# Kernel optimization log

Hardware: AMD Instinct MI355X
Metric: run time of the kernel (lower is better)

Reference implementation:

```python
import jax, jax.numpy as jnp
import numpy as np
from jax import lax

L, T, DM, DH = 4, 4096, 2048, 1024
MAX_PHASE = 6.28
EPS = 1e-5


def setup_inputs() -> dict:
    key = jax.random.key(0)
    ks = jax.random.split(key, 16)
    # LRU initializers (r_min=0, r_max=1)
    u1 = jax.random.uniform(ks[0], (L, DH))
    nu_log = jnp.log(-0.5 * jnp.log(u1))
    u2 = jax.random.uniform(ks[1], (L, DH))
    theta_log = jnp.log(MAX_PHASE * u2)
    abs_lam = jnp.exp(-jnp.exp(nu_log))  # |lambda|
    gamma_log = jnp.log(jnp.sqrt(1.0 - abs_lam ** 2))
    B_re = jax.random.normal(ks[2], (L, DH, DM)) / np.sqrt(2 * DM)
    B_im = jax.random.normal(ks[3], (L, DH, DM)) / np.sqrt(2 * DM)
    C_re = jax.random.normal(ks[4], (L, DM, DH)) / np.sqrt(DH)
    C_im = jax.random.normal(ks[5], (L, DM, DH)) / np.sqrt(DH)
    D = jax.random.normal(ks[6], (L, DM))
    bound = 1.0 / np.sqrt(DM)
    enc_w = jax.random.uniform(ks[7], (DM, DM), minval=-bound, maxval=bound)
    enc_b = jax.random.uniform(ks[8], (DM,), minval=-bound, maxval=bound)
    out1_w = jax.random.uniform(ks[9], (L, DM, DM), minval=-bound, maxval=bound)
    out1_b = jax.random.uniform(ks[10], (L, DM), minval=-bound, maxval=bound)
    out2_w = jax.random.uniform(ks[11], (L, DM, DM), minval=-bound, maxval=bound)
    out2_b = jax.random.uniform(ks[12], (L, DM), minval=-bound, maxval=bound)
    norm_w = jnp.ones((L, DM))
    norm_b = jnp.zeros((L, DM))
    x = jax.random.normal(ks[13], (T, DM))
    return dict(x=x, enc_w=enc_w, enc_b=enc_b, nu_log=nu_log, theta_log=theta_log,
                gamma_log=gamma_log, B_re=B_re, B_im=B_im, C_re=C_re, C_im=C_im,
                D=D, norm_w=norm_w, norm_b=norm_b, out1_w=out1_w, out1_b=out1_b,
                out2_w=out2_w, out2_b=out2_b)


def _lru(xn, nu, th, gl, br, bi, cr, ci, d):
    # xn: (T, DM) real -> (T, DM) real
    lam = jnp.exp(-jnp.exp(nu) + 1j * jnp.exp(th))          # (DH,) complex
    B_norm = (br + 1j * bi) * jnp.exp(gl)[:, None]           # (DH, DM)
    Bu = xn.astype(B_norm.dtype) @ B_norm.T                  # (T, DH) complex
    a = jnp.broadcast_to(lam, Bu.shape)
    def combine(e1, e2):
        a1, b1 = e1
        a2, b2 = e2
        return a1 * a2, a2 * b1 + b2
    _, h = lax.associative_scan(combine, (a, Bu), axis=0)    # h_t = lam*h_{t-1} + Bu_t
    C = cr + 1j * ci
    return (h @ C.T).real + xn * d


def _batchnorm(x, w, b):
    # training-mode BatchNorm1d over dim 0 (biased variance), matching torch
    mu = x.mean(axis=0)
    var = jnp.mean((x - mu) ** 2, axis=0)
    return (x - mu) / jnp.sqrt(var + EPS) * w + b


def _forward(x, enc_w, enc_b, nu_log, theta_log, gamma_log, B_re, B_im,
             C_re, C_im, D, norm_w, norm_b, out1_w, out1_b, out2_w, out2_b):
    x = x @ enc_w.T + enc_b
    def layer(carry, p):
        nu, th, gl, br, bi, cr, ci, d, nw, nb, w1, b1, w2, b2 = p
        xn = _batchnorm(carry, nw, nb)
        y = _lru(xn, nu, th, gl, br, bi, cr, ci, d)
        y = jax.nn.gelu(y, approximate=False)
        y = (y @ w1.T + b1) * jax.nn.sigmoid(y @ w2.T + b2)
        return carry + y, None
    x, _ = lax.scan(layer, x, (nu_log, theta_log, gamma_log, B_re, B_im,
                               C_re, C_im, D, norm_w, norm_b,
                               out1_w, out1_b, out2_w, out2_b))
    return x


def reference(x, enc_w, enc_b, nu_log, theta_log, gamma_log, B_re, B_im,
              C_re, C_im, D, norm_w, norm_b, out1_w, out1_b, out2_w, out2_b):
    return _forward(x, enc_w, enc_b, nu_log, theta_log, gamma_log, B_re, B_im,
                    C_re, C_im, D, norm_w, norm_b, out1_w, out1_b, out2_w, out2_b)
```

## Files before the change

kernel.cpp:

```cpp
#include <hip/hip_runtime.h>
#include <stdint.h>
#include <math.h>


#define LAYERS 4
#define TT     4096
#define DMODEL 2048
#define DHID   1024
#define NCHUNK 64
#define CLEN   64
#define KTILES 64

typedef unsigned short ushort_t;
typedef __attribute__((ext_vector_type(8))) _Float16 half8;
typedef __attribute__((ext_vector_type(4))) float    f32x4;

__device__ __forceinline__ unsigned pack2h(float a, float b) {
  _Float16 ha = (_Float16)a, hb = (_Float16)b;
  unsigned short ua = *(unsigned short*)&ha, ub = *(unsigned short*)&hb;
  return (unsigned)ua | ((unsigned)ub << 16);
}

__global__ __launch_bounds__(256)
void convert_h(const float* __restrict__ B0, const float* __restrict__ B1,
               int ldb, int NS, int KS, ushort_t* __restrict__ Hi)
{
  __shared__ float tile[128][33];
  const int mb  = blockIdx.x;
  const int kb  = blockIdx.y;
  const int tid = threadIdx.x;
  const int r0  = tid >> 3;
  const int c0  = (tid & 7) * 4;
#pragma unroll
  for (int rep = 0; rep < 4; ++rep) {
    const int rr = rep * 32 + r0;
    const int n  = mb * 128 + rr;
    const int k  = kb * 32 + c0;
    const float* bp; long idx;
    if (n >= NS)      { bp = B1; idx = (long)(n - NS) * ldb + k; }
    else if (k >= KS) { bp = B1; idx = (long)n * ldb + (k - KS); }
    else              { bp = B0; idx = (long)n * ldb + k; }
#pragma unroll
    for (int u = 0; u < 4; ++u) tile[rr][c0 + u] = bp[idx + u];
  }
  __syncthreads();
#pragma unroll
  for (int rep = 0; rep < 2; ++rep) {
    const int id2 = rep * 256 + tid;
    const int kg  = id2 >> 7;
    const int m   = id2 & 127;
    const long off = ((long)mb * KTILES + kb) * 4096 + (kg * 128 + m) * 8;
    unsigned hw[4];
#pragma unroll
    for (int p = 0; p < 4; ++p)
      hw[p] = pack2h(tile[m][kg * 8 + p * 2], tile[m][kg * 8 + p * 2 + 1]);
    *(uint4*)&Hi[off] = make_uint4(hw[0], hw[1], hw[2], hw[3]);
  }
}

__global__ __launch_bounds__(256)
void bn_convert(const float* __restrict__ carry, const float* __restrict__ stats,
                const float* __restrict__ nw, const float* __restrict__ nb,
                float* __restrict__ act, ushort_t* __restrict__ Hi)
{
  __shared__ float tile[128][33];
  const int mb  = blockIdx.x;
  const int kb  = blockIdx.y;
  const int tid = threadIdx.x;
  const int r0  = tid >> 3;
  const int c0  = (tid & 7) * 4;
  float mean[4], rstd[4], w_[4], b_[4];
#pragma unroll
  for (int u = 0; u < 4; ++u) {
    const int j = kb * 32 + c0 + u;
    const float mu = stats[j] * (1.0f / TT);
    const float va = fmaxf(stats[DMODEL + j] * (1.0f / TT) - mu * mu, 0.0f);
    mean[u] = mu; rstd[u] = rsqrtf(va + 1e-5f);
    w_[u] = nw[j]; b_[u] = nb[j];
  }
#pragma unroll
  for (int rep = 0; rep < 4; ++rep) {
    const int rr  = rep * 32 + r0;
    const long base = (long)(mb * 128 + rr) * 2048 + kb * 32 + c0;
#pragma unroll
    for (int u = 0; u < 4; ++u) {
      const float v = (carry[base + u] - mean[u]) * rstd[u] * w_[u] + b_[u];
      tile[rr][c0 + u] = v;
      act[base + u] = v;
    }
  }
  __syncthreads();
#pragma unroll
  for (int rep = 0; rep < 2; ++rep) {
    const int id2 = rep * 256 + tid;
    const int kg  = id2 >> 7;
    const int m   = id2 & 127;
    const long off = ((long)mb * KTILES + kb) * 4096 + (kg * 128 + m) * 8;
    unsigned hw[4];
#pragma unroll
    for (int p = 0; p < 4; ++p)
      hw[p] = pack2h(tile[m][kg * 8 + p * 2], tile[m][kg * 8 + p * 2 + 1]);
    *(uint4*)&Hi[off] = make_uint4(hw[0], hw[1], hw[2], hw[3]);
  }
}

__global__ __launch_bounds__(256)
void e1_convert(const float* __restrict__ y, const float* __restrict__ xn,
                const float* __restrict__ d, ushort_t* __restrict__ Hi)
{
  __shared__ float tile[128][33];
  const int mb  = blockIdx.x;
  const int kb  = blockIdx.y;
  const int tid = threadIdx.x;
  const int r0  = tid >> 3;
  const int c0  = (tid & 7) * 4;
  float dv[4];
#pragma unroll
  for (int u = 0; u < 4; ++u) dv[u] = d[kb * 32 + c0 + u];
#pragma unroll
  for (int rep = 0; rep < 4; ++rep) {
    const int rr  = rep * 32 + r0;
    const long base = (long)(mb * 128 + rr) * 2048 + kb * 32 + c0;
#pragma unroll
    for (int u = 0; u < 4; ++u) {
      const float v = y[base + u] + xn[base + u] * dv[u];
      tile[rr][c0 + u] = 0.5f * v * (1.0f + erff(v * 0.70710678118654752440f));
    }
  }
  __syncthreads();
#pragma unroll
  for (int rep = 0; rep < 2; ++rep) {
    const int id2 = rep * 256 + tid;
    const int kg  = id2 >> 7;
    const int m   = id2 & 127;
    const long off = ((long)mb * KTILES + kb) * 4096 + (kg * 128 + m) * 8;
    unsigned hw[4];
#pragma unroll
    for (int p = 0; p < 4; ++p)
      hw[p] = pack2h(tile[m][kg * 8 + p * 2], tile[m][kg * 8 + p * 2 + 1]);
    *(uint4*)&Hi[off] = make_uint4(hw[0], hw[1], hw[2], hw[3]);
  }
}

#define GLDS(gp, lp) __builtin_amdgcn_global_load_lds( \
    (__attribute__((address_space(1))) void*)(void*)(gp), \
    (__attribute__((address_space(3))) void*)(lp), 16, 0, 0)

__global__ __launch_bounds__(256)
void gemm_mfma(const ushort_t* __restrict__ Ahi, const ushort_t* __restrict__ Bhi,
               float* __restrict__ C, const float* __restrict__ bias,
               int epi, const float* __restrict__ aux)
{
  __shared__ ushort_t S[2][16384];
  const int tid  = threadIdx.x;
  const int lane = tid & 63;
  const int wid  = tid >> 6;
  const int wm   = wid >> 1;
  const int wn   = wid & 1;

  const int bid = blockIdx.y * gridDim.x + blockIdx.x;
  const int xcd = bid & 7, idx = bid >> 3;
  const int mb  = ((xcd & 3) << 3) | (idx & 7);
  const int nb  = ((xcd >> 2) << 3) | (idx >> 3);

  f32x4 acc[4][4];
#pragma unroll
  for (int i = 0; i < 4; ++i)
#pragma unroll
    for (int j = 0; j < 4; ++j) acc[i][j] = (f32x4){0.f, 0.f, 0.f, 0.f};

  const ushort_t* ga = Ahi + (long)mb * KTILES * 4096 + tid * 8;
  const ushort_t* gb = Bhi + (long)nb * KTILES * 4096 + tid * 8;

  const int albase = ((lane >> 4) * 128 + wm * 64 + (lane & 15)) * 8;
  const int blbase = ((lane >> 4) * 128 + wn * 64 + (lane & 15)) * 8;

  half8 A0[4], B0[4], A1[4], B1[4];

#define STAGE(P) \
  GLDS(ga,        &S[P][tid * 8]); \
  GLDS(ga + 2048, &S[P][2048 + tid * 8]); \
  GLDS(ga + 4096, &S[P][4096 + tid * 8]); \
  GLDS(ga + 6144, &S[P][6144 + tid * 8]); \
  GLDS(gb,        &S[P][8192 + tid * 8]); \
  GLDS(gb + 2048, &S[P][10240 + tid * 8]); \
  GLDS(gb + 4096, &S[P][12288 + tid * 8]); \
  GLDS(gb + 6144, &S[P][14336 + tid * 8]); \
  ga += 8192; gb += 8192;

#define RD(P) \
  _Pragma("unroll") \
  for (int m = 0; m < 4; ++m) A0[m] = *(const half8*)&S[P][albase + m * 128]; \
  _Pragma("unroll") \
  for (int n = 0; n < 4; ++n) B0[n] = *(const half8*)&S[P][8192 + blbase + n * 128]; \
  _Pragma("unroll") \
  for (int m = 0; m < 4; ++m) A1[m] = *(const half8*)&S[P][4096 + albase + m * 128]; \
  _Pragma("unroll") \
  for (int n = 0; n < 4; ++n) B1[n] = *(const half8*)&S[P][12288 + blbase + n * 128];

#define MFMA16(A_, B_) \
  _Pragma("unroll") \
  for (int m = 0; m < 4; ++m) \
    _Pragma("unroll") \
    for (int n = 0; n < 4; ++n) \
      acc[m][n] = __builtin_amdgcn_mfma_f32_16x16x32_f16(A_[m], B_[n], acc[m][n], 0, 0, 0);

#define WAIT_VM_BAR(n) asm volatile("s_waitcnt vmcnt(" #n ")" ::: "memory"); \
  __builtin_amdgcn_sched_barrier(0); __builtin_amdgcn_s_barrier();
#define LGKM0_BAR asm volatile("s_waitcnt lgkmcnt(0)" ::: "memory"); \
  __builtin_amdgcn_sched_barrier(0); __builtin_amdgcn_s_barrier();

#define KSTEP(P) \
  WAIT_VM_BAR(8) \
  RD(P) \
  __builtin_amdgcn_s_setprio(1); \
  MFMA16(A0, B0) \
  MFMA16(A1, B1) \
  __builtin_amdgcn_s_setprio(0); \
  LGKM0_BAR \
  STAGE(P)

  STAGE(0)
  STAGE(1)
  for (int it = 0; it < 15; ++it) {
    KSTEP(0)
    KSTEP(1)
  }
  WAIT_VM_BAR(8)
  RD(0)
  __builtin_amdgcn_s_setprio(1);
  MFMA16(A0, B0)
  MFMA16(A1, B1)
  __builtin_amdgcn_s_setprio(0);
  WAIT_VM_BAR(0)
  RD(1)
  __builtin_amdgcn_s_setprio(1);
  MFMA16(A0, B0)
  MFMA16(A1, B1)
  __builtin_amdgcn_s_setprio(0);
#undef STAGE
#undef RD
#undef MFMA16
#undef WAIT_VM_BAR
#undef LGKM0_BAR
#undef KSTEP

  const int cn = lane & 15;
  const int cr = (lane >> 4) * 4;
#pragma unroll
  for (int m = 0; m < 4; ++m) {
    const long row = (long)mb * 128 + wm * 64 + m * 16 + cr;
#pragma unroll
    for (int n = 0; n < 4; ++n) {
      const int col = nb * 128 + wn * 64 + n * 16 + cn;
      const float bv = bias ? bias[col] : 0.0f;
      if (epi == 0) {
#pragma unroll
        for (int q = 0; q < 4; ++q)
          C[(row + q) * 2048 + col] = acc[m][n][q] + bv;
      } else if (epi == 1) {
#pragma unroll
        for (int q = 0; q < 4; ++q)
          C[(row + q) * 2048 + col] = 1.0f / (1.0f + expf(-(acc[m][n][q] + bv)));
      } else {
#pragma unroll
        for (int q = 0; q < 4; ++q) {
          const long idx2 = (row + q) * 2048 + col;
          C[idx2] += (acc[m][n][q] + bv) * aux[idx2];
        }
      }
    }
  }
}

__global__ __launch_bounds__(256)
void gemm_dual(const ushort_t* __restrict__ Ahi, const ushort_t* __restrict__ B1t,
               const ushort_t* __restrict__ B2t,
               float* __restrict__ carry, const float* __restrict__ b1,
               const float* __restrict__ b2)
{
  __shared__ ushort_t S[3][8192];
  const int tid  = threadIdx.x;
  const int lane = tid & 63;
  const int wid  = tid >> 6;
  const int wm   = wid >> 1;
  const int wn   = wid & 1;

  const int bid = blockIdx.y * gridDim.x + blockIdx.x;
  const int xcd = bid & 7, idx = bid >> 3;
  const int mb  = ((xcd & 3) << 3) | (idx & 7);
  const int nbb = ((xcd >> 2) << 4) | (idx >> 3);

  f32x4 acc1[4][2], acc2[4][2];
#pragma unroll
  for (int i = 0; i < 4; ++i)
#pragma unroll
    for (int j = 0; j < 2; ++j) {
      acc1[i][j] = (f32x4){0.f, 0.f, 0.f, 0.f};
      acc2[i][j] = (f32x4){0.f, 0.f, 0.f, 0.f};
    }

  const int nt = nbb >> 1;
  const int hb = nbb & 1;

  const ushort_t* ga = Ahi + (long)mb * KTILES * 4096 + tid * 8;
  const long boff = ((tid >> 6) * 128 + hb * 64 + (tid & 63)) * 8;
  const ushort_t* g1 = B1t + (long)nt * KTILES * 4096 + boff;
  const ushort_t* g2 = B2t + (long)nt * KTILES * 4096 + boff;

  const int albase = ((lane >> 4) * 128 + wm * 64 + (lane & 15)) * 8;
  const int blbase = ((lane >> 4) * 64 + wn * 32 + (lane & 15)) * 8;

  half8 Af[4], B1f[2], B2f[2];

#define STAGE(P) \
  GLDS(ga,        &S[P][tid * 8]); \
  GLDS(ga + 2048, &S[P][2048 + tid * 8]); \
  GLDS(g1,        &S[P][4096 + tid * 8]); \
  GLDS(g2,        &S[P][6144 + tid * 8]); \
  ga += 4096; g1 += 4096; g2 += 4096;

#define RD(P) \
  _Pragma("unroll") \
  for (int m = 0; m < 4; ++m) Af[m]  = *(const half8*)&S[P][albase + m * 128]; \
  _Pragma("unroll") \
  for (int n = 0; n < 2; ++n) B1f[n] = *(const half8*)&S[P][4096 + blbase + n * 128]; \
  _Pragma("unroll") \
  for (int n = 0; n < 2; ++n) B2f[n] = *(const half8*)&S[P][6144 + blbase + n * 128];

#define MFMA16D \
  __builtin_amdgcn_s_setprio(1); \
  _Pragma("unroll") \
  for (int m = 0; m < 4; ++m) \
    _Pragma("unroll") \
    for (int n = 0; n < 2; ++n) \
      acc1[m][n] = __builtin_amdgcn_mfma_f32_16x16x32_f16(Af[m], B1f[n], acc1[m][n], 0, 0, 0); \
  _Pragma("unroll") \
  for (int m = 0; m < 4; ++m) \
    _Pragma("unroll") \
    for (int n = 0; n < 2; ++n) \
      acc2[m][n] = __builtin_amdgcn_mfma_f32_16x16x32_f16(Af[m], B2f[n], acc2[m][n], 0, 0, 0); \
  __builtin_amdgcn_s_setprio(0);

#define WAITB(n) asm volatile("s_waitcnt vmcnt(" #n ") lgkmcnt(0)" ::: "memory"); \
  __builtin_amdgcn_sched_barrier(0); __builtin_amdgcn_s_barrier();

#define KSTEPD(PRD, PST) \
  WAITB(4) \
  STAGE(PST) \
  RD(PRD) \
  MFMA16D

  STAGE(0)
  STAGE(1)

  for (int it = 0; it < 20; ++it) {
    KSTEPD(0, 2)
    KSTEPD(1, 0)
    KSTEPD(2, 1)
  }
  KSTEPD(0, 2)
  KSTEPD(1, 0)
  WAITB(4)
  RD(2)
  MFMA16D
  WAITB(0)
  RD(0)
  MFMA16D
#undef STAGE
#undef RD
#undef MFMA16D
#undef WAITB
#undef KSTEPD

  const int cn = lane & 15;
  const int cr = (lane >> 4) * 4;
#pragma unroll
  for (int m = 0; m < 4; ++m) {
    const long row = (long)mb * 128 + wm * 64 + m * 16 + cr;
#pragma unroll
    for (int n = 0; n < 2; ++n) {
      const int col = nbb * 64 + wn * 32 + n * 16 + cn;
      const float b1v = b1[col], b2v = b2[col];
#pragma unroll
      for (int q = 0; q < 4; ++q) {
        const long idx2 = (row + q) * 2048 + col;
        const float t1v = acc1[m][n][q] + b1v;
        const float t2v = acc2[m][n][q] + b2v;
        carry[idx2] += t1v * (1.0f / (1.0f + expf(-t2v)));
      }
    }
  }
}

__global__ void bn_partial(const float* __restrict__ carry, float* __restrict__ stats)
{
  const int j  = blockIdx.x * 256 + threadIdx.x;
  const int r0 = blockIdx.y * 128;
  float s = 0.f, ss = 0.f;
  for (int r = 0; r < 128; ++r) {
    float v = carry[(long)(r0 + r) * DMODEL + j];
    s += v; ss += v * v;
  }
  atomicAdd(&stats[j], s);
  atomicAdd(&stats[DMODEL + j], ss);
}

__device__ __forceinline__ void get_lam(const float* nu_log, const float* th_log,
                                        int h, float& lre, float& lim)
{
  const float mag = expf(-expf(nu_log[h]));
  const float th  = expf(th_log[h]);
  lre = mag * cosf(th);
  lim = mag * sinf(th);
}

__global__ void scan1(float* __restrict__ bu,
                      const float* __restrict__ nu_log, const float* __restrict__ th_log,
                      const float* __restrict__ gl_log)
{
  const int gid = blockIdx.x * 256 + threadIdx.x;
  const int c = gid >> 10, h = gid & 1023;
  float lre, lim; get_lam(nu_log, th_log, h, lre, lim);
  const float gamma = expf(gl_log[h]);
  float hr = 0.f, hi = 0.f;
  for (int i = 0; i < CLEN; ++i) {
    const long t = (long)c * CLEN + i;
    const float br_ = bu[t * 2048 + h] * gamma;
    const float bi_ = bu[t * 2048 + 1024 + h] * gamma;
    const float nr = lre * hr - lim * hi + br_;
    const float ni = lre * hi + lim * hr + bi_;
    hr = nr; hi = ni;
    bu[t * 2048 + h] = hr;
    bu[t * 2048 + 1024 + h] = hi;
  }
}

__global__ void scan2(const float* __restrict__ loc,
                      float* __restrict__ ccre, float* __restrict__ ccim,
                      const float* __restrict__ nu_log, const float* __restrict__ th_log)
{
  const int h = blockIdx.x * 256 + threadIdx.x;
  float lre, lim; get_lam(nu_log, th_log, h, lre, lim);
  float ar = lre, ai = lim;
  for (int s = 0; s < 6; ++s) { float nr = ar * ar - ai * ai, ni = 2.f * ar * ai; ar = nr; ai = ni; }
  float er = 0.f, ei = 0.f;
  for (int c = 0; c < NCHUNK; ++c) {
    ccre[c * DHID + h] = er; ccim[c * DHID + h] = ei;
    const long t = (long)c * CLEN + (CLEN - 1);
    const float nr = ar * er - ai * ei + loc[t * 2048 + h];
    const float ni = ar * ei + ai * er + loc[t * 2048 + 1024 + h];
    er = nr; ei = ni;
  }
}

__global__ void scan3(float* __restrict__ loc,
                      const float* __restrict__ ccre, const float* __restrict__ ccim,
                      const float* __restrict__ nu_log, const float* __restrict__ th_log)
{
  const int gid = blockIdx.x * 256 + threadIdx.x;
  const int c = gid >> 10, h = gid & 1023;
  float lre, lim; get_lam(nu_log, th_log, h, lre, lim);
  const float cr_ = ccre[c * DHID + h], ci_ = ccim[c * DHID + h];
  float pr = lre, pi = lim;
  for (int i = 0; i < CLEN; ++i) {
    const long t = (long)c * CLEN + i;
    const float hre = loc[t * 2048 + h]        + pr * cr_ - pi * ci_;
    const float him = loc[t * 2048 + 1024 + h] + pr * ci_ + pi * cr_;
    const float npr = pr * lre - pi * lim, npi = pr * lim + pi * lre;
    pr = npr; pi = npi;
    loc[t * 2048 + h]        = hre;
    loc[t * 2048 + 1024 + h] = -him;
  }
}

__global__ void finalize(const float* __restrict__ carry, float* __restrict__ out)
{
  const long idx = (long)blockIdx.x * 256 + threadIdx.x;
  const float v = carry[idx];
  out[idx] = (v == v && fabsf(v) < 3.0e38f) ? v : 300000.0f;
}

__global__ void diagfill(float* __restrict__ out, float val)
{
  const long idx = (long)blockIdx.x * 256 + threadIdx.x;
  out[idx] = (idx == 0) ? val : 0.0f;
}

extern "C" void kernel_launch(void* const* d_in, const int* in_sizes, int n_in,
                              void* d_out, int out_size, void* d_ws, size_t ws_size,
                              hipStream_t stream)
{
  (void)out_size;
  const int EW = (TT * DMODEL) / 256;
  float* out = (float*)d_out;

  if (n_in != 17 || in_sizes[0] != TT * DMODEL) {
    diagfill<<<EW, 256, 0, stream>>>(out, (float)(1 << 18));
    return;
  }
  if (ws_size < 151600000ull) {
    diagfill<<<EW, 256, 0, stream>>>(out, (float)(1 << 12));
    return;
  }

  const float* x     = (const float*)d_in[0];
  const float* enc_w = (const float*)d_in[1];
  const float* enc_b = (const float*)d_in[2];
  const float* nu    = (const float*)d_in[3];
  const float* th    = (const float*)d_in[4];
  const float* gl    = (const float*)d_in[5];
  const float* Bre   = (const float*)d_in[6];
  const float* Bim   = (const float*)d_in[7];
  const float* Cre   = (const float*)d_in[8];
  const float* Cim   = (const float*)d_in[9];
  const float* Dd    = (const float*)d_in[10];
  const float* nw    = (const float*)d_in[11];
  const float* nb    = (const float*)d_in[12];
  const float* w1    = (const float*)d_in[13];
  const float* b1    = (const float*)d_in[14];
  const float* w2    = (const float*)d_in[15];
  const float* b2    = (const float*)d_in[16];

  char* ws = (char*)d_ws;
  float*    carry = (float*)(ws);
  float*    act   = (float*)(ws + 33554432);
  float*    buf1  = (float*)(ws + 67108864);
  ushort_t* Ahi   = (ushort_t*)(ws + 100663296);
  ushort_t* B2hi  = (ushort_t*)(ws + 117440512);
  ushort_t* Bhi   = (ushort_t*)(ws + 134217728);
  float*    ccre  = (float*)(ws + 150994944);
  float*    ccim  = (float*)(ws + 151257088);
  float*    stats = (float*)(ws + 151519232);

  const dim3 gcA(32, 64);
  const dim3 gcW(16, 64);
  const dim3 gg(32, 16);
  const dim3 gg2(32, 32);
  const int BIG = 1 << 30;

  convert_h<<<gcA, 256, 0, stream>>>(x, x, 2048, BIG, BIG, Ahi);
  convert_h<<<gcW, 256, 0, stream>>>(enc_w, enc_w, 2048, BIG, BIG, Bhi);
  gemm_mfma<<<gg, 256, 0, stream>>>(Ahi, Bhi, carry, enc_b, 0, nullptr);

  for (int l = 0; l < LAYERS; ++l) {
    const float* Brl = Bre + (size_t)l * DHID * DMODEL;
    const float* Bil = Bim + (size_t)l * DHID * DMODEL;
    const float* Crl = Cre + (size_t)l * DMODEL * DHID;
    const float* Cil = Cim + (size_t)l * DMODEL * DHID;
    const float* w1l = w1 + (size_t)l * DMODEL * DMODEL;
    const float* w2l = w2 + (size_t)l * DMODEL * DMODEL;

    hipMemsetAsync(stats, 0, 2 * DMODEL * sizeof(float), stream);
    bn_partial<<<dim3(DMODEL / 256, TT / 128), 256, 0, stream>>>(carry, stats);
    bn_convert<<<gcA, 256, 0, stream>>>(carry, stats, nw + l * DMODEL, nb + l * DMODEL,
                                        act, Ahi);

    convert_h<<<gcW, 256, 0, stream>>>(Brl, Bil, 2048, 1024, BIG, Bhi);
    gemm_mfma<<<gg, 256, 0, stream>>>(Ahi, Bhi, buf1, nullptr, 0, nullptr);

    scan1<<<256, 256, 0, stream>>>(buf1, nu + l * DHID, th + l * DHID, gl + l * DHID);
    scan2<<<4, 256, 0, stream>>>(buf1, ccre, ccim, nu + l * DHID, th + l * DHID);
    scan3<<<256, 256, 0, stream>>>(buf1, ccre, ccim, nu + l * DHID, th + l * DHID);

    convert_h<<<gcA, 256, 0, stream>>>(buf1, buf1, 2048, BIG, BIG, Ahi);
    convert_h<<<gcW, 256, 0, stream>>>(Crl, Cil, 1024, BIG, 1024, Bhi);
    gemm_mfma<<<gg, 256, 0, stream>>>(Ahi, Bhi, buf1, nullptr, 0, nullptr);

    e1_convert<<<gcA, 256, 0, stream>>>(buf1, act, Dd + l * DMODEL, Ahi);

    convert_h<<<gcW, 256, 0, stream>>>(w1l, w1l, 2048, BIG, BIG, Bhi);
    convert_h<<<gcW, 256, 0, stream>>>(w2l, w2l, 2048, BIG, BIG, B2hi);
    gemm_dual<<<gg2, 256, 0, stream>>>(Ahi, Bhi, B2hi, carry,
                                       b1 + l * DMODEL, b2 + l * DMODEL);
  }

  finalize<<<EW, 256, 0, stream>>>(carry, out);
}
```

Baseline: 1.404 ms.

## Fuse BN stats into GEMM epilogues and scan fix-up into fp16 conversion

Per-column sum and sum-of-squares for batch norm are now accumulated in the epilogues of the encoder GEMM and the dual output GEMM, via LDS then global atomics, which removes the separate bn_partial pass over carry. The scan3 carry fix-up is folded into a new scan3_convert kernel that computes lambda^p in closed form with exp and sincos and writes fp16 GEMM tiles directly, dropping one fp32 read/write pass and one convert_h. The normalized activation is kept only as the fp16 tiled copy, so the skip term D*xn reads half-precision data instead of an fp32 act buffer. The costs are lower precision on the skip term, a fast __sincosf evaluated at angles up to several hundred radians, and extra atomics in the GEMM epilogues.

New measurement: 1.307 ms. 1.07x faster.

```diff
diff --git a/kernel.cpp b/kernel.cpp
--- a/kernel.cpp
+++ b/kernel.cpp
@@ -61,7 +61,7 @@
 __global__ __launch_bounds__(256)
 void bn_convert(const float* __restrict__ carry, const float* __restrict__ stats,
                 const float* __restrict__ nw, const float* __restrict__ nb,
-                float* __restrict__ act, ushort_t* __restrict__ Hi)
+                ushort_t* __restrict__ Hi)
 {
   __shared__ float tile[128][33];
   const int mb  = blockIdx.x;
@@ -83,11 +83,8 @@
     const int rr  = rep * 32 + r0;
     const long base = (long)(mb * 128 + rr) * 2048 + kb * 32 + c0;
 #pragma unroll
-    for (int u = 0; u < 4; ++u) {
-      const float v = (carry[base + u] - mean[u]) * rstd[u] * w_[u] + b_[u];
-      tile[rr][c0 + u] = v;
-      act[base + u] = v;
-    }
+    for (int u = 0; u < 4; ++u)
+      tile[rr][c0 + u] = (carry[base + u] - mean[u]) * rstd[u] * w_[u] + b_[u];
   }
   __syncthreads();
 #pragma unroll
@@ -105,8 +102,10 @@
 }
 
 __global__ __launch_bounds__(256)
-void e1_convert(const float* __restrict__ y, const float* __restrict__ xn,
-                const float* __restrict__ d, ushort_t* __restrict__ Hi)
+void scan3_convert(const float* __restrict__ loc,
+                   const float* __restrict__ ccre, const float* __restrict__ ccim,
+                   const float* __restrict__ nu_log, const float* __restrict__ th_log,
+                   ushort_t* __restrict__ Hi)
 {
   __shared__ float tile[128][33];
   const int mb  = blockIdx.x;
@@ -114,17 +113,39 @@
   const int tid = threadIdx.x;
   const int r0  = tid >> 3;
   const int c0  = (tid & 7) * 4;
-  float dv[4];
-#pragma unroll
-  for (int u = 0; u < 4; ++u) dv[u] = d[kb * 32 + c0 + u];
+  const int isim = (kb >= 32);
+  const int c0l  = (mb * 2) & 1023;
+  (void)c0l;
+  float en[4], eth[4], cr0[4], ci0[4], cr1[4], ci1[4];
+#pragma unroll
+  for (int u = 0; u < 4; ++u) {
+    const int col = kb * 32 + c0 + u;
+    const int h   = col & 1023;
+    en[u]  = expf(nu_log[h]);
+    eth[u] = expf(th_log[h]);
+    const int ch0 = mb * 2, ch1 = mb * 2 + 1;
+    cr0[u] = ccre[ch0 * DHID + h]; ci0[u] = ccim[ch0 * DHID + h];
+    cr1[u] = ccre[ch1 * DHID + h]; ci1[u] = ccim[ch1 * DHID + h];
+  }
 #pragma unroll
   for (int rep = 0; rep < 4; ++rep) {
     const int rr  = rep * 32 + r0;
+    const int sel = rr >> 6;
+    const float p = (float)((rr & 63) + 1);
     const long base = (long)(mb * 128 + rr) * 2048 + kb * 32 + c0;
 #pragma unroll
     for (int u = 0; u < 4; ++u) {
-      const float v = y[base + u] + xn[base + u] * dv[u];
-      tile[rr][c0 + u] = 0.5f * v * (1.0f + erff(v * 0.70710678118654752440f));
+      const float magp = expf(-p * en[u]);
+      const float ang  = p * eth[u];
+      float sv, cv;
+      __sincosf(ang, &sv, &cv);
+      const float pr = magp * cv, pi = magp * sv;
+      const float cr_ = sel ? cr1[u] : cr0[u];
+      const float ci_ = sel ? ci1[u] : ci0[u];
+      const float L = loc[base + u];
+      const float v = isim ? -(L + pr * ci_ + pi * cr_)
+                           :  (L + pr * cr_ - pi * ci_);
+      tile[rr][c0 + u] = v;
     }
   }
   __syncthreads();
@@ -136,8 +157,50 @@
     const long off = ((long)mb * KTILES + kb) * 4096 + (kg * 128 + m) * 8;
     unsigned hw[4];
 #pragma unroll
-    for (int p = 0; p < 4; ++p)
-      hw[p] = pack2h(tile[m][kg * 8 + p * 2], tile[m][kg * 8 + p * 2 + 1]);
+    for (int p2 = 0; p2 < 4; ++p2)
+      hw[p2] = pack2h(tile[m][kg * 8 + p2 * 2], tile[m][kg * 8 + p2 * 2 + 1]);
+    *(uint4*)&Hi[off] = make_uint4(hw[0], hw[1], hw[2], hw[3]);
+  }
+}
+
+__global__ __launch_bounds__(256)
+void e1_convert(const float* __restrict__ y, const ushort_t* __restrict__ xnT,
+                const float* __restrict__ d, ushort_t* __restrict__ Hi)
+{
+  __shared__ float tile[128][33];
+  const int mb  = blockIdx.x;
+  const int kb  = blockIdx.y;
+  const int tid = threadIdx.x;
+  const int r0  = tid >> 3;
+  const int c0  = (tid & 7) * 4;
+#pragma unroll
+  for (int rep = 0; rep < 4; ++rep) {
+    const int rr  = rep * 32 + r0;
+    const long base = (long)(mb * 128 + rr) * 2048 + kb * 32 + c0;
+#pragma unroll
+    for (int u = 0; u < 4; ++u) tile[rr][c0 + u] = y[base + u];
+  }
+  __syncthreads();
+#pragma unroll
+  for (int rep = 0; rep < 2; ++rep) {
+    const int id2 = rep * 256 + tid;
+    const int kg  = id2 >> 7;
+    const int m   = id2 & 127;
+    const long off = ((long)mb * KTILES + kb) * 4096 + (kg * 128 + m) * 8;
+    const half8 xh = *(const half8*)&xnT[off];
+    const float* dp = d + kb * 32 + kg * 8;
+    unsigned hw[4];
+#pragma unroll
+    for (int p = 0; p < 4; ++p) {
+      float g2[2];
+#pragma unroll
+      for (int e = 0; e < 2; ++e) {
+        const int j = p * 2 + e;
+        const float v = tile[m][kg * 8 + j] + (float)xh[j] * dp[j];
+        g2[e] = 0.5f * v * (1.0f + erff(v * 0.70710678118654752440f));
+      }
+      hw[p] = pack2h(g2[0], g2[1]);
+    }
     *(uint4*)&Hi[off] = make_uint4(hw[0], hw[1], hw[2], hw[3]);
   }
 }
@@ -149,7 +212,7 @@
 __global__ __launch_bounds__(256)
 void gemm_mfma(const ushort_t* __restrict__ Ahi, const ushort_t* __restrict__ Bhi,
                float* __restrict__ C, const float* __restrict__ bias,
-               int epi, const float* __restrict__ aux)
+               int epi, float* __restrict__ stats)
 {
   __shared__ ushort_t S[2][16384];
   const int tid  = threadIdx.x;
@@ -247,6 +310,7 @@
 
   const int cn = lane & 15;
   const int cr = (lane >> 4) * 4;
+  float s0[4] = {0.f, 0.f, 0.f, 0.f}, s1[4] = {0.f, 0.f, 0.f, 0.f};
 #pragma unroll
   for (int m = 0; m < 4; ++m) {
     const long row = (long)mb * 128 + wm * 64 + m * 16 + cr;
@@ -256,19 +320,33 @@
       const float bv = bias ? bias[col] : 0.0f;
       if (epi == 0) {
 #pragma unroll
+        for (int q = 0; q < 4; ++q) {
+          const float v = acc[m][n][q] + bv;
+          C[(row + q) * 2048 + col] = v;
+          s0[n] += v; s1[n] += v * v;
+        }
+      } else {
+#pragma unroll
         for (int q = 0; q < 4; ++q)
           C[(row + q) * 2048 + col] = acc[m][n][q] + bv;
-      } else if (epi == 1) {
-#pragma unroll
-        for (int q = 0; q < 4; ++q)
-          C[(row + q) * 2048 + col] = 1.0f / (1.0f + expf(-(acc[m][n][q] + bv)));
-      } else {
-#pragma unroll
-        for (int q = 0; q < 4; ++q) {
-          const long idx2 = (row + q) * 2048 + col;
-          C[idx2] += (acc[m][n][q] + bv) * aux[idx2];
-        }
       }
+    }
+  }
+  if (stats) {
+    __syncthreads();
+    float* sred = (float*)&S[0][0];
+    if (tid < 256) sred[tid] = 0.f;
+    __syncthreads();
+#pragma unroll
+    for (int n = 0; n < 4; ++n) {
+      const int lc = wn * 64 + n * 16 + cn;
+      atomicAdd(&sred[lc], s0[n]);
+      atomicAdd(&sred[128 + lc], s1[n]);
+    }
+    __syncthreads();
+    if (tid < 128) {
+      atomicAdd(&stats[nb * 128 + tid], sred[tid]);
+      atomicAdd(&stats[DMODEL + nb * 128 + tid], sred[128 + tid]);
     }
   }
 }
@@ -277,7 +355,7 @@
 void gemm_dual(const ushort_t* __restrict__ Ahi, const ushort_t* __restrict__ B1t,
                const ushort_t* __restrict__ B2t,
                float* __restrict__ carry, const float* __restrict__ b1,
-               const float* __restrict__ b2)
+               const float* __restrict__ b2, float* __restrict__ stats)
 {
   __shared__ ushort_t S[3][8192];
   const int tid  = threadIdx.x;
@@ -353,7 +431,6 @@
 
   STAGE(0)
   STAGE(1)
-
   for (int it = 0; it < 20; ++it) {
     KSTEPD(0, 2)
     KSTEPD(1, 0)
@@ -375,6 +452,7 @@
 
   const int cn = lane & 15;
   const int cr = (lane >> 4) * 4;
+  float s0[2] = {0.f, 0.f}, s1[2] = {0.f, 0.f};
 #pragma unroll
   for (int m = 0; m < 4; ++m) {
     const long row = (long)mb * 128 + wm * 64 + m * 16 + cr;
@@ -387,23 +465,29 @@
         const long idx2 = (row + q) * 2048 + col;
         const float t1v = acc1[m][n][q] + b1v;
         const float t2v = acc2[m][n][q] + b2v;
-        carry[idx2] += t1v * (1.0f / (1.0f + expf(-t2v)));
+        const float v = carry[idx2] + t1v * (1.0f / (1.0f + expf(-t2v)));
+        carry[idx2] = v;
+        s0[n] += v; s1[n] += v * v;
       }
     }
   }
-}
-
-__global__ void bn_partial(const float* __restrict__ carry, float* __restrict__ stats)
-{
-  const int j  = blockIdx.x * 256 + threadIdx.x;
-  const int r0 = blockIdx.y * 128;
-  float s = 0.f, ss = 0.f;
-  for (int r = 0; r < 128; ++r) {
-    float v = carry[(long)(r0 + r) * DMODEL + j];
-    s += v; ss += v * v;
-  }
-  atomicAdd(&stats[j], s);
-  atomicAdd(&stats[DMODEL + j], ss);
+  if (stats) {
+    __syncthreads();
+    float* sred = (float*)&S[0][0];
+    if (tid < 128) sred[tid] = 0.f;
+    __syncthreads();
+#pragma unroll
+    for (int n = 0; n < 2; ++n) {
+      const int lc = wn * 32 + n * 16 + cn;
+      atomicAdd(&sred[lc], s0[n]);
+      atomicAdd(&sred[64 + lc], s1[n]);
+    }
+    __syncthreads();
+    if (tid < 64) {
+      atomicAdd(&stats[nbb * 64 + tid], sred[tid]);
+      atomicAdd(&stats[DMODEL + nbb * 64 + tid], sred[64 + tid]);
+    }
+  }
 }
 
 __device__ __forceinline__ void get_lam(const float* nu_log, const float* th_log,
@@ -451,26 +535,6 @@
     const float nr = ar * er - ai * ei + loc[t * 2048 + h];
     const float ni = ar * ei + ai * er + loc[t * 2048 + 1024 + h];
     er = nr; ei = ni;
-  }
-}
-
-__global__ void scan3(float* __restrict__ loc,
-                      const float* __restrict__ ccre, const float* __restrict__ ccim,
-                      const float* __restrict__ nu_log, const float* __restrict__ th_log)
-{
-  const int gid = blockIdx.x * 256 + threadIdx.x;
-  const int c = gid >> 10, h = gid & 1023;
-  float lre, lim; get_lam(nu_log, th_log, h, lre, lim);
-  const float cr_ = ccre[c * DHID + h], ci_ = ccim[c * DHID + h];
-  float pr = lre, pi = lim;
-  for (int i = 0; i < CLEN; ++i) {
-    const long t = (long)c * CLEN + i;
-    const float hre = loc[t * 2048 + h]        + pr * cr_ - pi * ci_;
-    const float him = loc[t * 2048 + 1024 + h] + pr * ci_ + pi * cr_;
-    const float npr = pr * lre - pi * lim, npi = pr * lim + pi * lre;
-    pr = npr; pi = npi;
-    loc[t * 2048 + h]        = hre;
-    loc[t * 2048 + 1024 + h] = -him;
   }
 }
 
@@ -524,7 +588,7 @@
 
   char* ws = (char*)d_ws;
   float*    carry = (float*)(ws);
-  float*    act   = (float*)(ws + 33554432);
+  ushort_t* AhiX  = (ushort_t*)(ws + 33554432);
   float*    buf1  = (float*)(ws + 67108864);
   ushort_t* Ahi   = (ushort_t*)(ws + 100663296);
   ushort_t* B2hi  = (ushort_t*)(ws + 117440512);
@@ -539,9 +603,10 @@
   const dim3 gg2(32, 32);
   const int BIG = 1 << 30;
 
+  hipMemsetAsync(stats, 0, 2 * DMODEL * sizeof(float), stream);
   convert_h<<<gcA, 256, 0, stream>>>(x, x, 2048, BIG, BIG, Ahi);
   convert_h<<<gcW, 256, 0, stream>>>(enc_w, enc_w, 2048, BIG, BIG, Bhi);
-  gemm_mfma<<<gg, 256, 0, stream>>>(Ahi, Bhi, carry, enc_b, 0, nullptr);
+  gemm_mfma<<<gg, 256, 0, stream>>>(Ahi, Bhi, carry, enc_b, 0, stats);
 
   for (int l = 0; l < LAYERS; ++l) {
     const float* Brl = Bre + (size_t)l * DHID * DMODEL;
@@ -551,28 +616,29 @@
     const float* w1l = w1 + (size_t)l * DMODEL * DMODEL;
     const float* w2l = w2 + (size_t)l * DMODEL * DMODEL;
 
-    hipMemsetAsync(stats, 0, 2 * DMODEL * sizeof(float), stream);
-    bn_partial<<<dim3(DMODEL / 256, TT / 128), 256, 0, stream>>>(carry, stats);
-    bn_convert<<<gcA, 256, 0, stream>>>(carry, stats, nw + l * DMODEL, nb + l * DMODEL,
-                                        act, Ahi);
+    bn_convert<<<gcA, 256, 0, stream>>>(carry, stats, nw + l * DMODEL,
+                                        nb + l * DMODEL, AhiX);
 
     convert_h<<<gcW, 256, 0, stream>>>(Brl, Bil, 2048, 1024, BIG, Bhi);
-    gemm_mfma<<<gg, 256, 0, stream>>>(Ahi, Bhi, buf1, nullptr, 0, nullptr);
+    gemm_mfma<<<gg, 256, 0, stream>>>(AhiX, Bhi, buf1, nullptr, 3, nullptr);
 
     scan1<<<256, 256, 0, stream>>>(buf1, nu + l * DHID, th + l * DHID, gl + l * DHID);
     scan2<<<4, 256, 0, stream>>>(buf1, ccre, ccim, nu + l * DHID, th + l * DHID);
-    scan3<<<256, 256, 0, stream>>>(buf1, ccre, ccim, nu + l * DHID, th + l * DHID);
-
-    convert_h<<<gcA, 256, 0, stream>>>(buf1, buf1, 2048, BIG, BIG, Ahi);
+
     convert_h<<<gcW, 256, 0, stream>>>(Crl, Cil, 1024, BIG, 1024, Bhi);
-    gemm_mfma<<<gg, 256, 0, stream>>>(Ahi, Bhi, buf1, nullptr, 0, nullptr);
-
-    e1_convert<<<gcA, 256, 0, stream>>>(buf1, act, Dd + l * DMODEL, Ahi);
+    scan3_convert<<<gcA, 256, 0, stream>>>(buf1, ccre, ccim, nu + l * DHID,
+                                           th + l * DHID, Ahi);
+
+    gemm_mfma<<<gg, 256, 0, stream>>>(Ahi, Bhi, buf1, nullptr, 3, nullptr);
+
+    e1_convert<<<gcA, 256, 0, stream>>>(buf1, AhiX, Dd + l * DMODEL, Ahi);
 
     convert_h<<<gcW, 256, 0, stream>>>(w1l, w1l, 2048, BIG, BIG, Bhi);
     convert_h<<<gcW, 256, 0, stream>>>(w2l, w2l, 2048, BIG, BIG, B2hi);
+    float* nstats = (l < LAYERS - 1) ? stats : nullptr;
+    if (nstats) hipMemsetAsync(stats, 0, 2 * DMODEL * sizeof(float), stream);
     gemm_dual<<<gg2, 256, 0, stream>>>(Ahi, Bhi, B2hi, carry,
-                                       b1 + l * DMODEL, b2 + l * DMODEL);
+                                       b1 + l * DMODEL, b2 + l * DMODEL, nstats);
   }
 
   finalize<<<EW, 256, 0, stream>>>(carry, out);
```
